# Optimization experiments

Hardware: AMD Instinct MI355X
Metric: run time of the kernel (lower is better)

The kernel has to match this reference:

```python
import jax, jax.numpy as jnp
import numpy as np

T_SEG = 8      # n_segment
KSZ = 3        # LAM temporal kernel size
PAD = 1        # LAM temporal padding
BN_EPS = 1e-5


def setup_inputs() -> dict:
    key = jax.random.key(0)
    ks = jax.random.split(key, 12)
    n, t, c, h, w = 8, T_SEG, 256, 56, 56
    return {
        "x": jax.random.normal(ks[0], (n * t, c, h, w), jnp.float32),
        "net_w": jax.random.normal(ks[1], (c, c, 3, 3), jnp.float32) * 0.02,
        "net_b": jax.random.normal(ks[2], (c,), jnp.float32) * 0.02,
        "lam_w": jax.random.normal(ks[3], (c, c), jnp.float32) * 0.02,
        "lam_b": jax.random.normal(ks[4], (c,), jnp.float32) * 0.02,
        "mlp_w1": jax.random.normal(ks[5], (2 * t, t), jnp.float32) * 0.3,
        "bn_gamma": jax.random.uniform(ks[6], (2 * t,), jnp.float32, 0.5, 1.5),
        "bn_beta": jax.random.normal(ks[7], (2 * t,), jnp.float32) * 0.1,
        "bn_mean": jax.random.normal(ks[8], (2 * t,), jnp.float32) * 0.1,
        "bn_var": jax.random.uniform(ks[9], (2 * t,), jnp.float32, 0.5, 1.5),
        "mlp_w2": jax.random.normal(ks[10], (KSZ, 2 * t), jnp.float32) * 0.3,
        "me_w": jax.random.normal(ks[11], (3,), jnp.float32) * 0.3,
    }


def reference(x, net_w, net_b, lam_w, lam_b, mlp_w1, bn_gamma, bn_beta,
              bn_mean, bn_var, mlp_w2, me_w):
    t = T_SEG
    nt, c, h, w = x.shape
    n = nt // t

    # --- wrapped net: Conv2d 3x3, pad 1 ---
    out = jax.lax.conv_general_dilated(
        x, net_w, window_strides=(1, 1), padding="SAME",
        dimension_numbers=("NCHW", "OIHW", "NCHW"))
    out = out + net_b[None, :, None, None]

    # --- LAM ---
    new_x = out.reshape(n, t, c, h, w).transpose(0, 2, 1, 3, 4)  # (n,c,t,h,w)
    x_g = new_x.mean(axis=(2, 3, 4))                   # global pool -> (n,c)
    x_g = x_g @ lam_w.T + lam_b                        # Conv1d k=1 == matmul
    new_x = new_x + x_g[:, :, None, None, None]

    pooled = new_x.mean(axis=(3, 4)).reshape(n * c, t)  # per-(n,c) temporal sig
    hdn = pooled @ mlp_w1.T                              # (n*c, 2t), no bias
    hdn = (hdn - bn_mean) * (bn_gamma / jnp.sqrt(bn_var + BN_EPS)) + bn_beta
    hdn = jax.nn.relu(hdn)
    wgt = jax.nn.softmax(hdn @ mlp_w2.T, axis=-1).reshape(n, c, KSZ)

    # grouped conv2d (groups=n*c) == per-(n,c) depthwise temporal conv
    xpad = jnp.pad(new_x, ((0, 0), (0, 0), (PAD, PAD), (0, 0), (0, 0)))
    lam_out = sum(wgt[:, :, k, None, None, None] * xpad[:, :, k:k + t]
                  for k in range(KSZ))                  # (n,c,t,h,w)
    lam_out = lam_out.transpose(0, 2, 1, 3, 4).reshape(nt, c, h, w)

    # --- ME ---
    xv = lam_out.reshape(n, t, c, h, w)
    diff = xv[:, 1:] - xv[:, :-1]                       # frame differences
    diff = jnp.pad(diff, ((0, 0), (0, 1), (0, 0), (0, 0), (0, 0)))
    diff = diff.reshape(nt, c, h, w)
    y = diff.mean(axis=(2, 3))                          # (nt, c)
    ypad = jnp.pad(y, ((0, 0), (1, 1)))                 # conv1d over channel dim
    yc = sum(me_w[k] * ypad[:, k:k + c] for k in range(3))
    gate = jax.nn.sigmoid(yc)[:, :, None, None]

    return gate * lam_out
```

## Files before the change

### kernel.cpp

```cpp
#include <hip/hip_runtime.h>
#include <hip/hip_bf16.h>
#include <stdint.h>

#define AS1 __attribute__((address_space(1)))
#define AS3 __attribute__((address_space(3)))

typedef __attribute__((ext_vector_type(8))) short short8v;
typedef __attribute__((ext_vector_type(4))) float float4v;

#define NT 64
#define CCH 256
#define HH 56
#define WW 56
#define HWSZ 3136
#define HP 58
#define WP 58

#define OFF_XT   0ull
#define SZ_XT    110231552ull
#define OFF_WPK  (OFF_XT + SZ_XT)
#define SZ_WPK   1179648ull
#define OFF_CS   (OFF_WPK + SZ_WPK)
#define SZ_CS    65536ull
#define OFF_XG2  (OFF_CS + SZ_CS)
#define SZ_XG2   8192ull
#define OFF_WGT  (OFF_XG2 + SZ_XG2)
#define SZ_WGT   24576ull
#define OFF_M    (OFF_WGT + SZ_WGT)
#define SZ_M     65536ull
#define OFF_GATE (OFF_M + SZ_M)
#define SZ_GATE  65536ull

__device__ __forceinline__ unsigned short f2bf(float f) {
    unsigned int u = __float_as_uint(f);
    unsigned int r = (u + 0x7fffu + ((u >> 16) & 1u)) >> 16;
    return (unsigned short)r;
}

__device__ __forceinline__ void gload16(const unsigned short* g, unsigned short* l) {
    __builtin_amdgcn_global_load_lds((const AS1 void*)g, (AS3 void*)l, 16, 0, 0);
}

__global__ __launch_bounds__(256) void k0_transpose(const float* __restrict__ x,
                                                    unsigned short* __restrict__ xt) {
    int b = blockIdx.x;
    int cb = b & 3;
    int h  = (b >> 2) % 56;
    int nt = b / (4 * 56);
    int c0 = cb * 64;
    int tid = threadIdx.x;

    __shared__ float xs[64 * 57];

    const float* src = x + ((size_t)nt * CCH + c0) * HWSZ + h * WW;
    for (int li = tid; li < 896; li += 256) {
        int row = li / 14, f4 = li % 14;
        float4v v = *(const float4v*)(src + (size_t)row * HWSZ + f4 * 4);
        float* d = &xs[row * 57 + f4 * 4];
        d[0] = v.x; d[1] = v.y; d[2] = v.z; d[3] = v.w;
    }
    __syncthreads();

    unsigned short* dst = xt + (((size_t)nt * HP + (h + 1)) * WP) * CCH + c0;
    for (int job = tid; job < 464; job += 256) {
        int ww = job >> 3, cg = job & 7;
        short8v v;
        if (ww == 0 || ww == 57) {
            v = (short8v){0,0,0,0,0,0,0,0};
        } else {
            #pragma unroll
            for (int jj = 0; jj < 8; ++jj)
                v[jj] = (short)f2bf(xs[(cg * 8 + jj) * 57 + (ww - 1)]);
        }
        *(short8v*)(dst + ww * CCH + cg * 8) = v;
    }
    if (h == 0) {
        unsigned short* d0  = xt + ((size_t)nt * HP + 0)  * WP * CCH + c0;
        unsigned short* d57 = xt + ((size_t)nt * HP + 57) * WP * CCH + c0;
        short8v z = (short8v){0,0,0,0,0,0,0,0};
        for (int job = tid; job < 464; job += 256) {
            int ww = job >> 3, cg = job & 7;
            *(short8v*)(d0  + ww * CCH + cg * 8) = z;
            *(short8v*)(d57 + ww * CCH + cg * 8) = z;
        }
    }
}

__global__ __launch_bounds__(256) void kw_pack(const float* __restrict__ nw,
                                               unsigned short* __restrict__ wpk) {
    int idx = blockIdx.x * 256 + threadIdx.x;
    int rs = idx >> 16;
    int k  = (idx >> 8) & 255;
    int c  = idx & 255;
    wpk[idx] = f2bf(nw[(k * 256 + c) * 9 + rs]);
}


#define STGALL(bi_, tA_, tB_) do { \
    gload16(wpk + (tA_) + aoffg0, &lds[(bi_) * 8192 + ldsa0]); \
    gload16(wpk + (tA_) + aoffg1, &lds[(bi_) * 8192 + ldsa1]); \
    gload16(xt  + (tB_) + boffg,  &lds[24576 + (bi_) * 4096 + ldsb]); \
} while (0)

#define LDAF(mi) (*(const short8v*)&lds[abase + (wm * 64 + (mi) * 16 + r16) * 32 + pA * 8])
#define LDBF(j)  (*(const short8v*)&lds[bbase + (wp * 64 + (j) * 16 + r16) * 32 + pA * 8])

#define BARSYNC do { \
    __builtin_amdgcn_s_barrier(); \
    __builtin_amdgcn_sched_barrier(0); \
} while (0)

__global__ __launch_bounds__(512, 4) void conv_mfma(const unsigned short* __restrict__ xt,
                                                    const unsigned short* __restrict__ wpk,
                                                    const float* __restrict__ net_b,
                                                    float* __restrict__ out,
                                                    float* __restrict__ chansum) {
    __shared__ unsigned short lds[36864];

    const int tid  = threadIdx.x;
    const int lane = tid & 63;
    const int wid  = tid >> 6;
    const int wm   = wid >> 1;
    const int wp   = wid & 1;
    const int r16  = lane & 15;
    const int hi   = lane >> 4;
    const int pA   = (hi + (r16 >> 1)) & 3;

    const int pb0 = (blockIdx.x & 7) * 192 + (blockIdx.x >> 3);

    const int cgs = ((tid & 3) - (tid >> 3)) & 3;
    const int aoffg0 = (tid >> 2) * 256 + cgs * 8;
    const int aoffg1 = aoffg0 + 32768;
    const int ldsa0  = tid * 8;
    const int ldsa1  = ldsa0 + 4096;
    const int ldsb   = tid * 8;

    for (int g = pb0; g < 1568; g += 1536) {
        const int p0 = g * 128;

        long boffg;
        {
            int r = tid >> 2;
            int p = p0 + r;
            int nt = p / HWSZ, hw = p - nt * HWSZ;
            int hh = hw / WW,  w  = hw - hh * WW;
            boffg = ((long)(nt * HP + hh) * WP + w) * 256 + cgs * 8;
        }

        float4v acc[4][4];
        #pragma unroll
        for (int i = 0; i < 4; ++i)
            #pragma unroll
            for (int j = 0; j < 4; ++j) acc[i][j] = (float4v){0.f, 0.f, 0.f, 0.f};

        STGALL(0, 0, 0);
        STGALL(1, 32, 32);

        int cur = 0;
        for (int kt = 0; kt < 72; ++kt) {
            const int abase = cur * 8192;
            const int bbase = 24576 + cur * 4096;

            if (kt < 70) {
                const int ktn = kt + 2;
                int nb2 = cur + 2; if (nb2 >= 3) nb2 -= 3;
                const int rsn = ktn >> 3, con = (ktn & 7) * 32;
                const int tAn = rsn * 65536 + con;
                const int tBn = ((rsn / 3) * WP + (rsn - (rsn / 3) * 3)) * 256 + con;
                STGALL(nb2, tAn, tBn);
                asm volatile("s_waitcnt vmcnt(6)" ::: "memory");
            } else if (kt == 70) {
                asm volatile("s_waitcnt vmcnt(3)" ::: "memory");
            } else {
                asm volatile("s_waitcnt vmcnt(0)" ::: "memory");
            }
            BARSYNC;

            short8v afrag[4], bfrag[4];
            #pragma unroll
            for (int mi = 0; mi < 4; ++mi) afrag[mi] = LDAF(mi);
            #pragma unroll
            for (int j = 0; j < 4; ++j) bfrag[j] = LDBF(j);

            asm volatile("s_waitcnt lgkmcnt(0)" ::: "memory");
            __builtin_amdgcn_sched_barrier(0);
            __builtin_amdgcn_s_setprio(1);
            #pragma unroll
            for (int j = 0; j < 4; ++j)
                #pragma unroll
                for (int mi = 0; mi < 4; ++mi)
                    acc[mi][j] = __builtin_amdgcn_mfma_f32_16x16x32_bf16(afrag[mi], bfrag[j], acc[mi][j], 0, 0, 0);
            __builtin_amdgcn_s_setprio(0);
            BARSYNC;

            ++cur; if (cur >= 3) cur = 0;
        }

        const int pw = p0 + wp * 64;
        const int ntw = pw / HWSZ;
        const int hwb = pw - ntw * HWSZ;
        #pragma unroll
        for (int mi = 0; mi < 4; ++mi) {
            #pragma unroll
            for (int r = 0; r < 4; ++r) {
                const int m = wm * 64 + mi * 16 + hi * 4 + r;
                const float bias = net_b[m];
                float csum = 0.f;
                float* orow = out + ((size_t)ntw * CCH + m) * HWSZ + hwb;
                #pragma unroll
                for (int j = 0; j < 4; ++j) {
                    float v = acc[mi][j][r] + bias;
                    orow[j * 16 + r16] = v;
                    csum += v;
                }
                csum += __shfl_xor(csum, 1);
                csum += __shfl_xor(csum, 2);
                csum += __shfl_xor(csum, 4);
                csum += __shfl_xor(csum, 8);
                if (r16 == 0) atomicAdd(&chansum[ntw * CCH + m], csum);
            }
        }
    }
}

__global__ __launch_bounds__(256) void k2_xg(const float* __restrict__ chansum,
                                             const float* __restrict__ lam_w,
                                             const float* __restrict__ lam_b,
                                             float* __restrict__ xg2) {
    int n = blockIdx.x, c = threadIdx.x;
    __shared__ float xs[256];
    float s = 0.f;
    #pragma unroll
    for (int t = 0; t < 8; ++t) s += chansum[(n * 8 + t) * CCH + c];
    xs[c] = s * (1.0f / (3136.f * 8.f));
    __syncthreads();
    float d = lam_b[c];
    const float* row = lam_w + c * 256;
    for (int cc = 0; cc < 256; ++cc) d += row[cc] * xs[cc];
    xg2[n * 256 + c] = d;
}

__global__ __launch_bounds__(256) void k3_wgt(const float* __restrict__ chansum,
                                              const float* __restrict__ xg2,
                                              const float* __restrict__ w1,
                                              const float* __restrict__ bg,
                                              const float* __restrict__ bb,
                                              const float* __restrict__ bm,
                                              const float* __restrict__ bv,
                                              const float* __restrict__ w2,
                                              float* __restrict__ wgt,
                                              float* __restrict__ mbuf) {
    int idx = blockIdx.x * 256 + threadIdx.x;
    int n = idx >> 8, c = idx & 255;
    float xg = xg2[idx];
    float p[8];
    #pragma unroll
    for (int t = 0; t < 8; ++t)
        p[t] = chansum[(n * 8 + t) * CCH + c] * (1.0f / 3136.f) + xg;
    float hd[16];
    #pragma unroll
    for (int j = 0; j < 16; ++j) {
        float s = 0.f;
        #pragma unroll
        for (int t = 0; t < 8; ++t) s += p[t] * w1[j * 8 + t];
        s = (s - bm[j]) * (bg[j] * rsqrtf(bv[j] + 1e-5f)) + bb[j];
        hd[j] = fmaxf(s, 0.f);
    }
    float lg[3];
    #pragma unroll
    for (int k = 0; k < 3; ++k) {
        float s = 0.f;
        #pragma unroll
        for (int j = 0; j < 16; ++j) s += hd[j] * w2[k * 16 + j];
        lg[k] = s;
    }
    float mx = fmaxf(fmaxf(lg[0], lg[1]), lg[2]);
    float e0 = expf(lg[0] - mx), e1 = expf(lg[1] - mx), e2 = expf(lg[2] - mx);
    float inv = 1.f / (e0 + e1 + e2);
    float wk[3] = {e0 * inv, e1 * inv, e2 * inv};
    #pragma unroll
    for (int k = 0; k < 3; ++k) wgt[idx * 3 + k] = wk[k];
    #pragma unroll
    for (int t = 0; t < 8; ++t) {
        float s = 0.f;
        #pragma unroll
        for (int k = 0; k < 3; ++k) {
            int tt = t + k - 1;
            if (tt >= 0 && tt < 8) s += wk[k] * p[tt];
        }
        mbuf[idx * 8 + t] = s;
    }
}

__global__ __launch_bounds__(256) void k4_gate(const float* __restrict__ mbuf,
                                               const float* __restrict__ me_w,
                                               float* __restrict__ gate) {
    int b = blockIdx.x;
    int n = b >> 3, t = b & 7;
    int c = threadIdx.x;
    __shared__ float y[256];
    float yv = 0.f;
    if (t < 7) yv = mbuf[(n * 256 + c) * 8 + t + 1] - mbuf[(n * 256 + c) * 8 + t];
    y[c] = yv;
    __syncthreads();
    float yc = me_w[1] * yv;
    if (c > 0)   yc += me_w[0] * y[c - 1];
    if (c < 255) yc += me_w[2] * y[c + 1];
    gate[b * 256 + c] = 1.f / (1.f + expf(-yc));
}

__global__ __launch_bounds__(256) void k5_final(float* __restrict__ out,
                                                const float* __restrict__ wgt,
                                                const float* __restrict__ xg2,
                                                const float* __restrict__ gate) {
    int tid = blockIdx.x * 256 + threadIdx.x;
    int hw4 = tid % 784;
    int nc = tid / 784;
    int n = nc >> 8, c = nc & 255;
    float w0 = wgt[nc * 3 + 0], w1 = wgt[nc * 3 + 1], w2 = wgt[nc * 3 + 2];
    float xg = xg2[nc];
    const size_t tstride = (size_t)CCH * HWSZ;
    size_t base = ((size_t)(n * 8) * CCH + c) * HWSZ + hw4 * 4;

    float4v o[8];
    #pragma unroll
    for (int t = 0; t < 8; ++t) o[t] = *(const float4v*)(out + base + t * tstride);

    #pragma unroll
    for (int t = 0; t < 8; ++t) {
        float g = gate[(n * 8 + t) * CCH + c];
        float4v lam;
        #pragma unroll
        for (int q = 0; q < 4; ++q) {
            float v = w1 * (o[t][q] + xg);
            if (t > 0) v += w0 * (o[t - 1][q] + xg);
            if (t < 7) v += w2 * (o[t + 1][q] + xg);
            lam[q] = g * v;
        }
        *(float4v*)(out + base + t * tstride) = lam;
    }
}

extern "C" void kernel_launch(void* const* d_in, const int* in_sizes, int n_in,
                              void* d_out, int out_size, void* d_ws, size_t ws_size,
                              hipStream_t stream) {
    const float* x      = (const float*)d_in[0];
    const float* net_w  = (const float*)d_in[1];
    const float* net_b  = (const float*)d_in[2];
    const float* lam_w  = (const float*)d_in[3];
    const float* lam_b  = (const float*)d_in[4];
    const float* mlp_w1 = (const float*)d_in[5];
    const float* bn_g   = (const float*)d_in[6];
    const float* bn_b   = (const float*)d_in[7];
    const float* bn_m   = (const float*)d_in[8];
    const float* bn_v   = (const float*)d_in[9];
    const float* mlp_w2 = (const float*)d_in[10];
    const float* me_w   = (const float*)d_in[11];
    float* out = (float*)d_out;

    char* ws = (char*)d_ws;
    unsigned short* xt  = (unsigned short*)(ws + OFF_XT);
    unsigned short* wpk = (unsigned short*)(ws + OFF_WPK);
    float* chansum = (float*)(ws + OFF_CS);
    float* xg2     = (float*)(ws + OFF_XG2);
    float* wgt     = (float*)(ws + OFF_WGT);
    float* mbuf    = (float*)(ws + OFF_M);
    float* gate    = (float*)(ws + OFF_GATE);

    hipMemsetAsync(chansum, 0, SZ_CS, stream);
    kw_pack<<<2304, 256, 0, stream>>>(net_w, wpk);
    k0_transpose<<<64 * 56 * 4, 256, 0, stream>>>(x, xt);
    conv_mfma<<<1536, 512, 0, stream>>>(xt, wpk, net_b, out, chansum);
    k2_xg<<<8, 256, 0, stream>>>(chansum, lam_w, lam_b, xg2);
    k3_wgt<<<8, 256, 0, stream>>>(chansum, xg2, mlp_w1, bn_g, bn_b, bn_m, bn_v, mlp_w2, wgt, mbuf);
    k4_gate<<<64, 256, 0, stream>>>(mbuf, me_w, gate);
    k5_final<<<6272, 256, 0, stream>>>(out, wgt, xg2, gate);
}
```

Before: 431.7 us.

## Prefetch next K-tile A fragments from LDS during current MFMA block

Restructures the conv implicit-GEMM main loop into a 2x-unrolled ping-pong over register sets AX/AY, so the A fragments for the next K-tile are read from LDS while the current tile's MFMAs run. Only the B fragments are waited on before compute, which is meant to hide LDS read latency behind the matrix ops. The vmcnt waits are also tightened so the next stage is complete before the barrier. In exchange it uses more VGPRs for the second fragment set, which may pressure occupancy at 512 threads x 4 waves, and it relies on careful LDS slot and barrier ordering.

```diff
diff --git a/kernel.cpp b/kernel.cpp
--- a/kernel.cpp
+++ b/kernel.cpp
@@ -102,12 +102,48 @@
     gload16(xt  + (tB_) + boffg,  &lds[24576 + (bi_) * 4096 + ldsb]); \
 } while (0)
 
-#define LDAF(mi) (*(const short8v*)&lds[abase + (wm * 64 + (mi) * 16 + r16) * 32 + pA * 8])
-#define LDBF(j)  (*(const short8v*)&lds[bbase + (wp * 64 + (j) * 16 + r16) * 32 + pA * 8])
+#define LDAF(sl_, mi) (*(const short8v*)&lds[(sl_) * 8192 + (wm * 64 + (mi) * 16 + r16) * 32 + pA * 8])
+#define LDBF(sl_, j)  (*(const short8v*)&lds[24576 + (sl_) * 4096 + (wp * 64 + (j) * 16 + r16) * 32 + pA * 8])
 
 #define BARSYNC do { \
     __builtin_amdgcn_s_barrier(); \
     __builtin_amdgcn_sched_barrier(0); \
+} while (0)
+
+#define VMW_(n) asm volatile("s_waitcnt vmcnt(" #n ")" ::: "memory")
+#define LGK_(n) asm volatile("s_waitcnt lgkmcnt(" #n ")" ::: "memory")
+
+#define TILE(t_, cur_, ACUR, ANXT, HAS2, HAS1, VMC) do { \
+    if (HAS2) { \
+        int s2 = (cur_) + 2; if (s2 >= 3) s2 -= 3; \
+        const int ktn2 = (t_) + 2; \
+        const int rs2 = ktn2 >> 3, co2 = (ktn2 & 7) * 32; \
+        STGALL(s2, rs2 * 65536 + co2, \
+               ((rs2 / 3) * WP + (rs2 - (rs2 / 3) * 3)) * 256 + co2); \
+    } \
+    VMW_(VMC); \
+    BARSYNC;                             \
+    short8v bfrag[4]; \
+    _Pragma("unroll") \
+    for (int j = 0; j < 4; ++j) bfrag[j] = LDBF((cur_), j); \
+    __builtin_amdgcn_sched_barrier(0);   \
+    if (HAS1) { \
+        int s1 = (cur_) + 1; if (s1 >= 3) s1 -= 3; \
+        _Pragma("unroll") \
+        for (int mi = 0; mi < 4; ++mi) ANXT[mi] = LDAF(s1, mi); \
+        LGK_(4);                         \
+    } else { \
+        LGK_(0); \
+    } \
+    __builtin_amdgcn_sched_barrier(0); \
+    __builtin_amdgcn_s_setprio(1); \
+    _Pragma("unroll") \
+    for (int j = 0; j < 4; ++j) \
+        _Pragma("unroll") \
+        for (int mi = 0; mi < 4; ++mi) \
+            acc[mi][j] = __builtin_amdgcn_mfma_f32_16x16x32_bf16(ACUR[mi], bfrag[j], acc[mi][j], 0, 0, 0); \
+    __builtin_amdgcn_s_setprio(0); \
+    BARSYNC;                             \
 } while (0)
 
 __global__ __launch_bounds__(512, 4) void conv_mfma(const unsigned short* __restrict__ xt,
@@ -153,48 +189,25 @@
             #pragma unroll
             for (int j = 0; j < 4; ++j) acc[i][j] = (float4v){0.f, 0.f, 0.f, 0.f};
 
+        short8v AX[4], AY[4];
+
         STGALL(0, 0, 0);
         STGALL(1, 32, 32);
+        VMW_(3);
+        BARSYNC;
+        #pragma unroll
+        for (int mi = 0; mi < 4; ++mi) AX[mi] = LDAF(0, mi);
 
         int cur = 0;
-        for (int kt = 0; kt < 72; ++kt) {
-            const int abase = cur * 8192;
-            const int bbase = 24576 + cur * 4096;
-
-            if (kt < 70) {
-                const int ktn = kt + 2;
-                int nb2 = cur + 2; if (nb2 >= 3) nb2 -= 3;
-                const int rsn = ktn >> 3, con = (ktn & 7) * 32;
-                const int tAn = rsn * 65536 + con;
-                const int tBn = ((rsn / 3) * WP + (rsn - (rsn / 3) * 3)) * 256 + con;
-                STGALL(nb2, tAn, tBn);
-                asm volatile("s_waitcnt vmcnt(6)" ::: "memory");
-            } else if (kt == 70) {
-                asm volatile("s_waitcnt vmcnt(3)" ::: "memory");
-            } else {
-                asm volatile("s_waitcnt vmcnt(0)" ::: "memory");
-            }
-            BARSYNC;
-
-            short8v afrag[4], bfrag[4];
-            #pragma unroll
-            for (int mi = 0; mi < 4; ++mi) afrag[mi] = LDAF(mi);
-            #pragma unroll
-            for (int j = 0; j < 4; ++j) bfrag[j] = LDBF(j);
-
-            asm volatile("s_waitcnt lgkmcnt(0)" ::: "memory");
-            __builtin_amdgcn_sched_barrier(0);
-            __builtin_amdgcn_s_setprio(1);
-            #pragma unroll
-            for (int j = 0; j < 4; ++j)
-                #pragma unroll
-                for (int mi = 0; mi < 4; ++mi)
-                    acc[mi][j] = __builtin_amdgcn_mfma_f32_16x16x32_bf16(afrag[mi], bfrag[j], acc[mi][j], 0, 0, 0);
-            __builtin_amdgcn_s_setprio(0);
-            BARSYNC;
-
-            ++cur; if (cur >= 3) cur = 0;
-        }
+        for (int t2 = 0; t2 < 70; t2 += 2) {
+            TILE(t2, cur, AX, AY, true, true, 3);
+            cur = (cur == 2) ? 0 : cur + 1;
+            TILE(t2 + 1, cur, AY, AX, true, true, 3);
+            cur = (cur == 2) ? 0 : cur + 1;
+        }
+        TILE(70, cur, AX, AY, false, true, 0);
+        cur = (cur == 2) ? 0 : cur + 1;
+        TILE(71, cur, AY, AX, false, false, 0);
 
         const int pw = p0 + wp * 64;
         const int ntw = pw / HWSZ;
```

Result: slower. 453.9 us (+5.1%).

## Persist conv blocks over three tiles and split-K the tail tiles with atomics

Applied to the files above, without the earlier changes.

The convolution now launches 512 persistent blocks that each process three full pixel tiles. The leftover 32 tiles are split along the reduction dimension across 16 blocks each and accumulated with float atomics into the output. A new kernel pre-fills those output regions and their channel sums with the bias. The aim is to remove the load-imbalance tail, at the cost of atomic traffic, lower resident block count, and nondeterministic summation order.

```diff
diff --git a/kernel.cpp b/kernel.cpp
--- a/kernel.cpp
+++ b/kernel.cpp
@@ -95,6 +95,22 @@
     wpk[idx] = f2bf(nw[(k * 256 + c) * 9 + rs]);
 }
 
+__global__ __launch_bounds__(256) void kinit(const float* __restrict__ net_b,
+                                             float* __restrict__ out,
+                                             float* __restrict__ chansum) {
+    int idx = blockIdx.x * 256 + threadIdx.x;
+    int m  = idx >> 12;
+    int pp = idx & 4095;
+    int p  = 196608 + pp;
+    int nt = p / HWSZ, hw = p - nt * HWSZ;
+    out[((size_t)nt * CCH + m) * HWSZ + hw] = net_b[m];
+    if (pp < 64) {
+        int pc = 196608 + pp * 64;
+        int img = pc / HWSZ;
+        atomicAdd(&chansum[img * CCH + m], 64.0f * net_b[m]);
+    }
+}
+
 
 #define STGALL(bi_, tA_, tB_) do { \
     gload16(wpk + (tA_) + aoffg0, &lds[(bi_) * 8192 + ldsa0]); \
@@ -104,6 +120,9 @@
 
 #define LDAF(mi) (*(const short8v*)&lds[abase + (wm * 64 + (mi) * 16 + r16) * 32 + pA * 8])
 #define LDBF(j)  (*(const short8v*)&lds[bbase + (wp * 64 + (j) * 16 + r16) * 32 + pA * 8])
+
+#define KTA(kt) ((((kt) >> 3) << 16) + (((kt) & 7) * 32))
+#define KTB(kt) (((((kt) >> 3) / 3) * WP + (((kt) >> 3) - (((kt) >> 3) / 3) * 3)) * 256 + (((kt) & 7) * 32))
 
 #define BARSYNC do { \
     __builtin_amdgcn_s_barrier(); \
@@ -126,7 +145,7 @@
     const int hi   = lane >> 4;
     const int pA   = (hi + (r16 >> 1)) & 3;
 
-    const int pb0 = (blockIdx.x & 7) * 192 + (blockIdx.x >> 3);
+    const int pb0 = (blockIdx.x & 7) * 64 + (blockIdx.x >> 3);
 
     const int cgs = ((tid & 3) - (tid >> 3)) & 3;
     const int aoffg0 = (tid >> 2) * 256 + cgs * 8;
@@ -135,7 +154,8 @@
     const int ldsa1  = ldsa0 + 4096;
     const int ldsb   = tid * 8;
 
-    for (int g = pb0; g < 1568; g += 1536) {
+    for (int gi = 0; gi < 3; ++gi) {
+        const int g = pb0 + gi * 512;
         const int p0 = g * 128;
 
         long boffg;
@@ -164,10 +184,7 @@
             if (kt < 70) {
                 const int ktn = kt + 2;
                 int nb2 = cur + 2; if (nb2 >= 3) nb2 -= 3;
-                const int rsn = ktn >> 3, con = (ktn & 7) * 32;
-                const int tAn = rsn * 65536 + con;
-                const int tBn = ((rsn / 3) * WP + (rsn - (rsn / 3) * 3)) * 256 + con;
-                STGALL(nb2, tAn, tBn);
+                STGALL(nb2, KTA(ktn), KTB(ktn));
                 asm volatile("s_waitcnt vmcnt(6)" ::: "memory");
             } else if (kt == 70) {
                 asm volatile("s_waitcnt vmcnt(3)" ::: "memory");
@@ -221,6 +238,92 @@
             }
         }
     }
+
+    {
+        const int tt  = pb0 >> 4;
+        const int p0  = (1536 + tt) * 128;
+        const int ks  = pb0 & 15;
+        const int k0  = (ks < 8) ? ks * 5 : 40 + (ks - 8) * 4;
+        const int klen = (ks < 8) ? 5 : 4;
+
+        long boffg;
+        {
+            int r = tid >> 2;
+            int p = p0 + r;
+            int nt = p / HWSZ, hw = p - nt * HWSZ;
+            int hh = hw / WW,  w  = hw - hh * WW;
+            boffg = ((long)(nt * HP + hh) * WP + w) * 256 + cgs * 8;
+        }
+
+        float4v acc[4][4];
+        #pragma unroll
+        for (int i = 0; i < 4; ++i)
+            #pragma unroll
+            for (int j = 0; j < 4; ++j) acc[i][j] = (float4v){0.f, 0.f, 0.f, 0.f};
+
+        STGALL(0, KTA(k0), KTB(k0));
+        STGALL(1, KTA(k0 + 1), KTB(k0 + 1));
+
+        int cur = 0;
+        for (int i = 0; i < klen; ++i) {
+            const int abase = cur * 8192;
+            const int bbase = 24576 + cur * 4096;
+            if (i + 2 < klen) {
+                int s2 = cur + 2; if (s2 >= 3) s2 -= 3;
+                const int ktn = k0 + i + 2;
+                STGALL(s2, KTA(ktn), KTB(ktn));
+                asm volatile("s_waitcnt vmcnt(6)" ::: "memory");
+            } else if (i + 1 < klen) {
+                asm volatile("s_waitcnt vmcnt(3)" ::: "memory");
+            } else {
+                asm volatile("s_waitcnt vmcnt(0)" ::: "memory");
+            }
+            BARSYNC;
+
+            short8v afrag[4], bfrag[4];
+            #pragma unroll
+            for (int mi = 0; mi < 4; ++mi) afrag[mi] = LDAF(mi);
+            #pragma unroll
+            for (int j = 0; j < 4; ++j) bfrag[j] = LDBF(j);
+
+            asm volatile("s_waitcnt lgkmcnt(0)" ::: "memory");
+            __builtin_amdgcn_sched_barrier(0);
+            __builtin_amdgcn_s_setprio(1);
+            #pragma unroll
+            for (int j = 0; j < 4; ++j)
+                #pragma unroll
+                for (int mi = 0; mi < 4; ++mi)
+                    acc[mi][j] = __builtin_amdgcn_mfma_f32_16x16x32_bf16(afrag[mi], bfrag[j], acc[mi][j], 0, 0, 0);
+            __builtin_amdgcn_s_setprio(0);
+            BARSYNC;
+
+            ++cur; if (cur >= 3) cur = 0;
+        }
+
+        const int pw = p0 + wp * 64;
+        const int ntw = pw / HWSZ;
+        const int hwb = pw - ntw * HWSZ;
+        #pragma unroll
+        for (int mi = 0; mi < 4; ++mi) {
+            #pragma unroll
+            for (int r = 0; r < 4; ++r) {
+                const int m = wm * 64 + mi * 16 + hi * 4 + r;
+                float csum = 0.f;
+                float* orow = out + ((size_t)ntw * CCH + m) * HWSZ + hwb;
+                #pragma unroll
+                for (int j = 0; j < 4; ++j) {
+                    float v = acc[mi][j][r];
+                    atomicAdd(&orow[j * 16 + r16], v);
+                    csum += v;
+                }
+                csum += __shfl_xor(csum, 1);
+                csum += __shfl_xor(csum, 2);
+                csum += __shfl_xor(csum, 4);
+                csum += __shfl_xor(csum, 8);
+                if (r16 == 0) atomicAdd(&chansum[ntw * CCH + m], csum);
+            }
+        }
+    }
 }
 
 __global__ __launch_bounds__(256) void k2_xg(const float* __restrict__ chansum,
@@ -369,8 +472,9 @@
 
     hipMemsetAsync(chansum, 0, SZ_CS, stream);
     kw_pack<<<2304, 256, 0, stream>>>(net_w, wpk);
+    kinit<<<4096, 256, 0, stream>>>(net_b, out, chansum);
     k0_transpose<<<64 * 56 * 4, 256, 0, stream>>>(x, xt);
-    conv_mfma<<<1536, 512, 0, stream>>>(xt, wpk, net_b, out, chansum);
+    conv_mfma<<<512, 512, 0, stream>>>(xt, wpk, net_b, out, chansum);
     k2_xg<<<8, 256, 0, stream>>>(chansum, lam_w, lam_b, xg2);
     k3_wgt<<<8, 256, 0, stream>>>(chansum, xg2, mlp_w1, bn_g, bn_b, bn_m, bn_v, mlp_w2, wgt, mbuf);
     k4_gate<<<64, 256, 0, stream>>>(mbuf, me_w, gate);
```

After: 546.7 us. 26.6% more time.

## Store conv output as bf16 intermediate and fuse small LAM/ME kernels

Applied to the files above, without the earlier changes.

The conv kernel can write its biased output as bf16 into a workspace buffer instead of fp32 into the output, and the final kernel reads bf16 back. This halves the round-trip traffic of the large intermediate. The path is taken only when the workspace is large enough, and it adds bf16 rounding error to the final result. The three small kernels (xg, weight MLP, gate) are also merged into one kernel, which removes launches and the mbuf buffer.

```diff
diff --git a/kernel.cpp b/kernel.cpp
--- a/kernel.cpp
+++ b/kernel.cpp
@@ -6,6 +6,7 @@
 #define AS3 __attribute__((address_space(3)))
 
 typedef __attribute__((ext_vector_type(8))) short short8v;
+typedef __attribute__((ext_vector_type(4))) unsigned short ushort4v;
 typedef __attribute__((ext_vector_type(4))) float float4v;
 
 #define NT 64
@@ -26,15 +27,18 @@
 #define SZ_XG2   8192ull
 #define OFF_WGT  (OFF_XG2 + SZ_XG2)
 #define SZ_WGT   24576ull
-#define OFF_M    (OFF_WGT + SZ_WGT)
-#define SZ_M     65536ull
-#define OFF_GATE (OFF_M + SZ_M)
+#define OFF_GATE (OFF_WGT + SZ_WGT)
 #define SZ_GATE  65536ull
+#define OFF_CVT  (OFF_GATE + SZ_GATE)
+#define SZ_CVT   102760448ull
 
 __device__ __forceinline__ unsigned short f2bf(float f) {
     unsigned int u = __float_as_uint(f);
     unsigned int r = (u + 0x7fffu + ((u >> 16) & 1u)) >> 16;
     return (unsigned short)r;
+}
+__device__ __forceinline__ float bf2f(unsigned short u) {
+    return __uint_as_float(((unsigned int)u) << 16);
 }
 
 __device__ __forceinline__ void gload16(const unsigned short* g, unsigned short* l) {
@@ -110,10 +114,12 @@
     __builtin_amdgcn_sched_barrier(0); \
 } while (0)
 
+template <int OB>
 __global__ __launch_bounds__(512, 4) void conv_mfma(const unsigned short* __restrict__ xt,
                                                     const unsigned short* __restrict__ wpk,
                                                     const float* __restrict__ net_b,
                                                     float* __restrict__ out,
+                                                    unsigned short* __restrict__ cvt,
                                                     float* __restrict__ chansum) {
     __shared__ unsigned short lds[36864];
 
@@ -206,11 +212,12 @@
                 const int m = wm * 64 + mi * 16 + hi * 4 + r;
                 const float bias = net_b[m];
                 float csum = 0.f;
-                float* orow = out + ((size_t)ntw * CCH + m) * HWSZ + hwb;
+                const size_t obase = ((size_t)ntw * CCH + m) * HWSZ + hwb;
                 #pragma unroll
                 for (int j = 0; j < 4; ++j) {
                     float v = acc[mi][j][r] + bias;
-                    orow[j * 16 + r16] = v;
+                    if (OB) cvt[obase + j * 16 + r16] = f2bf(v);
+                    else    out[obase + j * 16 + r16] = v;
                     csum += v;
                 }
                 csum += __shfl_xor(csum, 1);
@@ -223,93 +230,93 @@
     }
 }
 
-__global__ __launch_bounds__(256) void k2_xg(const float* __restrict__ chansum,
-                                             const float* __restrict__ lam_w,
-                                             const float* __restrict__ lam_b,
-                                             float* __restrict__ xg2) {
+__global__ __launch_bounds__(256) void k234(const float* __restrict__ chansum,
+                                            const float* __restrict__ lam_w,
+                                            const float* __restrict__ lam_b,
+                                            const float* __restrict__ mw1,
+                                            const float* __restrict__ bg,
+                                            const float* __restrict__ bb,
+                                            const float* __restrict__ bm,
+                                            const float* __restrict__ bv,
+                                            const float* __restrict__ mw2,
+                                            const float* __restrict__ me_w,
+                                            float* __restrict__ xg2,
+                                            float* __restrict__ wgt,
+                                            float* __restrict__ gate) {
     int n = blockIdx.x, c = threadIdx.x;
     __shared__ float xs[256];
+    __shared__ float yd[8][256];
+
     float s = 0.f;
     #pragma unroll
     for (int t = 0; t < 8; ++t) s += chansum[(n * 8 + t) * CCH + c];
     xs[c] = s * (1.0f / (3136.f * 8.f));
     __syncthreads();
-    float d = lam_b[c];
+
+    float xg = lam_b[c];
     const float* row = lam_w + c * 256;
-    for (int cc = 0; cc < 256; ++cc) d += row[cc] * xs[cc];
-    xg2[n * 256 + c] = d;
-}
-
-__global__ __launch_bounds__(256) void k3_wgt(const float* __restrict__ chansum,
-                                              const float* __restrict__ xg2,
-                                              const float* __restrict__ w1,
-                                              const float* __restrict__ bg,
-                                              const float* __restrict__ bb,
-                                              const float* __restrict__ bm,
-                                              const float* __restrict__ bv,
-                                              const float* __restrict__ w2,
-                                              float* __restrict__ wgt,
-                                              float* __restrict__ mbuf) {
-    int idx = blockIdx.x * 256 + threadIdx.x;
-    int n = idx >> 8, c = idx & 255;
-    float xg = xg2[idx];
+    for (int cc = 0; cc < 256; ++cc) xg += row[cc] * xs[cc];
+    xg2[n * 256 + c] = xg;
+
     float p[8];
     #pragma unroll
     for (int t = 0; t < 8; ++t)
         p[t] = chansum[(n * 8 + t) * CCH + c] * (1.0f / 3136.f) + xg;
+
     float hd[16];
     #pragma unroll
     for (int j = 0; j < 16; ++j) {
-        float s = 0.f;
-        #pragma unroll
-        for (int t = 0; t < 8; ++t) s += p[t] * w1[j * 8 + t];
-        s = (s - bm[j]) * (bg[j] * rsqrtf(bv[j] + 1e-5f)) + bb[j];
-        hd[j] = fmaxf(s, 0.f);
+        float v = 0.f;
+        #pragma unroll
+        for (int t = 0; t < 8; ++t) v += p[t] * mw1[j * 8 + t];
+        v = (v - bm[j]) * (bg[j] * rsqrtf(bv[j] + 1e-5f)) + bb[j];
+        hd[j] = fmaxf(v, 0.f);
     }
     float lg[3];
     #pragma unroll
     for (int k = 0; k < 3; ++k) {
-        float s = 0.f;
-        #pragma unroll
-        for (int j = 0; j < 16; ++j) s += hd[j] * w2[k * 16 + j];
-        lg[k] = s;
+        float v = 0.f;
+        #pragma unroll
+        for (int j = 0; j < 16; ++j) v += hd[j] * mw2[k * 16 + j];
+        lg[k] = v;
     }
     float mx = fmaxf(fmaxf(lg[0], lg[1]), lg[2]);
     float e0 = expf(lg[0] - mx), e1 = expf(lg[1] - mx), e2 = expf(lg[2] - mx);
     float inv = 1.f / (e0 + e1 + e2);
     float wk[3] = {e0 * inv, e1 * inv, e2 * inv};
+    int idx = n * 256 + c;
     #pragma unroll
     for (int k = 0; k < 3; ++k) wgt[idx * 3 + k] = wk[k];
+
+    float mb[8];
     #pragma unroll
     for (int t = 0; t < 8; ++t) {
-        float s = 0.f;
+        float v = 0.f;
         #pragma unroll
         for (int k = 0; k < 3; ++k) {
             int tt = t + k - 1;
-            if (tt >= 0 && tt < 8) s += wk[k] * p[tt];
-        }
-        mbuf[idx * 8 + t] = s;
-    }
-}
-
-__global__ __launch_bounds__(256) void k4_gate(const float* __restrict__ mbuf,
-                                               const float* __restrict__ me_w,
-                                               float* __restrict__ gate) {
-    int b = blockIdx.x;
-    int n = b >> 3, t = b & 7;
-    int c = threadIdx.x;
-    __shared__ float y[256];
-    float yv = 0.f;
-    if (t < 7) yv = mbuf[(n * 256 + c) * 8 + t + 1] - mbuf[(n * 256 + c) * 8 + t];
-    y[c] = yv;
+            if (tt >= 0 && tt < 8) v += wk[k] * p[tt];
+        }
+        mb[t] = v;
+    }
+    #pragma unroll
+    for (int t = 0; t < 7; ++t) yd[t][c] = mb[t + 1] - mb[t];
+    yd[7][c] = 0.f;
     __syncthreads();
-    float yc = me_w[1] * yv;
-    if (c > 0)   yc += me_w[0] * y[c - 1];
-    if (c < 255) yc += me_w[2] * y[c + 1];
-    gate[b * 256 + c] = 1.f / (1.f + expf(-yc));
-}
-
+
+    float w0 = me_w[0], w1v = me_w[1], w2v = me_w[2];
+    #pragma unroll
+    for (int t = 0; t < 8; ++t) {
+        float yc = w1v * yd[t][c];
+        if (c > 0)   yc += w0 * yd[t][c - 1];
+        if (c < 255) yc += w2v * yd[t][c + 1];
+        gate[(n * 8 + t) * CCH + c] = 1.f / (1.f + expf(-yc));
+    }
+}
+
+template <int OB>
 __global__ __launch_bounds__(256) void k5_final(float* __restrict__ out,
+                                                const unsigned short* __restrict__ cvt,
                                                 const float* __restrict__ wgt,
                                                 const float* __restrict__ xg2,
                                                 const float* __restrict__ gate) {
@@ -324,7 +331,15 @@
 
     float4v o[8];
     #pragma unroll
-    for (int t = 0; t < 8; ++t) o[t] = *(const float4v*)(out + base + t * tstride);
+    for (int t = 0; t < 8; ++t) {
+        if (OB) {
+            ushort4v v = *(const ushort4v*)(cvt + base + t * tstride);
+            #pragma unroll
+            for (int q = 0; q < 4; ++q) o[t][q] = bf2f(v[q]);
+        } else {
+            o[t] = *(const float4v*)(out + base + t * tstride);
+        }
+    }
 
     #pragma unroll
     for (int t = 0; t < 8; ++t) {
@@ -364,15 +379,22 @@
     float* chansum = (float*)(ws + OFF_CS);
     float* xg2     = (float*)(ws + OFF_XG2);
     float* wgt     = (float*)(ws + OFF_WGT);
-    float* mbuf    = (float*)(ws + OFF_M);
     float* gate    = (float*)(ws + OFF_GATE);
+    unsigned short* cvt = (unsigned short*)(ws + OFF_CVT);
+
+    const bool use_bf16 = (ws_size >= OFF_CVT + SZ_CVT);
 
     hipMemsetAsync(chansum, 0, SZ_CS, stream);
     kw_pack<<<2304, 256, 0, stream>>>(net_w, wpk);
     k0_transpose<<<64 * 56 * 4, 256, 0, stream>>>(x, xt);
-    conv_mfma<<<1536, 512, 0, stream>>>(xt, wpk, net_b, out, chansum);
-    k2_xg<<<8, 256, 0, stream>>>(chansum, lam_w, lam_b, xg2);
-    k3_wgt<<<8, 256, 0, stream>>>(chansum, xg2, mlp_w1, bn_g, bn_b, bn_m, bn_v, mlp_w2, wgt, mbuf);
-    k4_gate<<<64, 256, 0, stream>>>(mbuf, me_w, gate);
-    k5_final<<<6272, 256, 0, stream>>>(out, wgt, xg2, gate);
-}
+    if (use_bf16)
+        conv_mfma<1><<<1536, 512, 0, stream>>>(xt, wpk, net_b, out, cvt, chansum);
+    else
+        conv_mfma<0><<<1536, 512, 0, stream>>>(xt, wpk, net_b, out, cvt, chansum);
+    k234<<<8, 256, 0, stream>>>(chansum, lam_w, lam_b, mlp_w1, bn_g, bn_b, bn_m, bn_v,
+                                mlp_w2, me_w, xg2, wgt, gate);
+    if (use_bf16)
+        k5_final<1><<<6272, 256, 0, stream>>>(out, cvt, wgt, xg2, gate);
+    else
+        k5_final<0><<<6272, 256, 0, stream>>>(out, cvt, wgt, xg2, gate);
+}
```

Result: faster. 412.5 us (-4.4%).
